# Kernel optimization log

Hardware: AMD Instinct MI355X
Metric: run time of the kernel (lower is better)

Reference implementation:

```python
import jax, jax.numpy as jnp
import numpy as np

N, E, G = 50000, 800000, 1024
IN, HID, H, L = 128, 128, 4, 3
C = HID // H  # per-head channels = 32
NEG_SLOPE = 0.2
BN_EPS = 1e-5


def setup_inputs() -> dict:
    key = jax.random.key(0)
    ks = jax.random.split(key, 12)
    s = 0.05
    x = jax.random.normal(ks[0], (N, IN), dtype=jnp.float32)
    edge_index = jax.random.randint(ks[1], (2, E), 0, N, dtype=jnp.int32)
    batch = jnp.sort(jax.random.randint(ks[2], (N,), 0, G, dtype=jnp.int32))
    # GATConv params per layer (in_dim == hidden_dim so all layers stack)
    Ws = jax.random.normal(ks[3], (L, HID, HID), dtype=jnp.float32) * s
    att_src = jax.random.normal(ks[4], (L, H, C), dtype=jnp.float32) * s
    att_dst = jax.random.normal(ks[5], (L, H, C), dtype=jnp.float32) * s
    biases = jax.random.normal(ks[6], (L, HID), dtype=jnp.float32) * s
    gammas = jnp.ones((L, HID), dtype=jnp.float32)
    betas = jnp.zeros((L, HID), dtype=jnp.float32)
    lin1_w = jax.random.normal(ks[7], (HID, HID // 2), dtype=jnp.float32) * s
    lin1_b = jnp.zeros((HID // 2,), dtype=jnp.float32)
    lin2_w = jax.random.normal(ks[8], (HID // 2, 1), dtype=jnp.float32) * s
    lin2_b = jnp.zeros((1,), dtype=jnp.float32)
    return dict(x=x, edge_index=edge_index, batch=batch, Ws=Ws, att_src=att_src,
                att_dst=att_dst, biases=biases, gammas=gammas, betas=betas,
                lin1_w=lin1_w, lin1_b=lin1_b, lin2_w=lin2_w, lin2_b=lin2_b)


def _gat_layer(x, src, dst, W, a_src, a_dst, bias):
    h = (x @ W).reshape(N, H, C)                      # [N,H,C]
    e_src = jnp.einsum('nhc,hc->nh', h, a_src)        # [N,H]
    e_dst = jnp.einsum('nhc,hc->nh', h, a_dst)
    e = jax.nn.leaky_relu(e_src[src] + e_dst[dst], NEG_SLOPE)  # [E',H]
    m = jax.ops.segment_max(e, dst, num_segments=N)   # segment softmax over dst
    ex = jnp.exp(e - m[dst])
    den = jax.ops.segment_sum(ex, dst, num_segments=N)
    alpha = ex / (den[dst] + 1e-16)
    msg = h[src] * alpha[:, :, None]                  # [E',H,C]
    out = jax.ops.segment_sum(msg, dst, num_segments=N).reshape(N, HID)
    return out + bias


def reference(x, edge_index, batch, Ws, att_src, att_dst, biases, gammas, betas,
              lin1_w, lin1_b, lin2_w, lin2_b):
    loop = jnp.arange(N, dtype=edge_index.dtype)      # add_self_loops=True
    src = jnp.concatenate([edge_index[0], loop])
    dst = jnp.concatenate([edge_index[1], loop])
    for l in range(L):
        h = _gat_layer(x, src, dst, Ws[l], att_src[l], att_dst[l], biases[l])
        mean = h.mean(axis=0)                         # BatchNorm1d (batch stats)
        var = h.var(axis=0)
        h = (h - mean) / jnp.sqrt(var + BN_EPS) * gammas[l] + betas[l]
        x = jax.nn.elu(h)
    cnt = jax.ops.segment_sum(jnp.ones((N,), x.dtype), batch, num_segments=G)
    pooled = jax.ops.segment_sum(x, batch, num_segments=G) / jnp.maximum(cnt, 1.0)[:, None]
    h1 = jax.nn.relu(pooled @ lin1_w + lin1_b)
    return (h1 @ lin2_w + lin2_b)[:, 0]               # [G]
```

## Files before the change

### kernel.cpp

```cpp
#include <hip/hip_runtime.h>
#include <hip/hip_fp16.h>
#include <math.h>

#define NN 50000
#define EE 800000
#define GG 1024
#define HIDD 128
#define NHEAD 4
#define EPTOT (EE + NN)
#define NEG_SLOPE 0.2f
#define NB ((NN + 255) / 256)
#define NTILE (NN / 16)

#define BSHIFT 9
#define NBUK 98
#define PCHUNK 4096
#define BCAP 10240

typedef _Float16 f16x8 __attribute__((ext_vector_type(8)));
typedef float f32x4 __attribute__((ext_vector_type(4)));

__global__ void zero_kernel(float* __restrict__ p, int n) {
  int i = blockIdx.x * blockDim.x + threadIdx.x;
  if (i < n) p[i] = 0.f;
}

__global__ void count_kernel(const int* __restrict__ ei, int* __restrict__ deg) {
  int e = blockIdx.x * blockDim.x + threadIdx.x;
  if (e >= EPTOT) return;
  int d = (e < EE) ? ei[EE + e] : (e - EE);
  atomicAdd(&deg[d], 1);
}

__global__ __launch_bounds__(256) void degsum_kernel(const int* __restrict__ deg,
                                                     int* __restrict__ bsum) {
  __shared__ int sh[256];
  int i = blockIdx.x * 256 + threadIdx.x;
  sh[threadIdx.x] = (i < NN) ? deg[i] : 0;
  __syncthreads();
  for (int off = 128; off > 0; off >>= 1) {
    if (threadIdx.x < off) sh[threadIdx.x] += sh[threadIdx.x + off];
    __syncthreads();
  }
  if (threadIdx.x == 0) bsum[blockIdx.x] = sh[0];
}

__global__ __launch_bounds__(256) void scanb_kernel(const int* __restrict__ bsum,
                                                    int* __restrict__ boff,
                                                    int* __restrict__ rowptr) {
  __shared__ int sh[256];
  int t = threadIdx.x;
  int v = (t < NB) ? bsum[t] : 0;
  sh[t] = v;
  __syncthreads();
  for (int off = 1; off < 256; off <<= 1) {
    int u = (t >= off) ? sh[t - off] : 0;
    __syncthreads();
    sh[t] += u;
    __syncthreads();
  }
  if (t < NB) boff[t] = sh[t] - v;
  if (t == 255) rowptr[NN] = sh[255];
}

__global__ __launch_bounds__(256) void rowptr_kernel(const int* __restrict__ deg,
                                                     const int* __restrict__ boff,
                                                     int* __restrict__ rowptr) {
  __shared__ int sh[256];
  int t = threadIdx.x;
  int i = blockIdx.x * 256 + t;
  int v = (i < NN) ? deg[i] : 0;
  sh[t] = v;
  __syncthreads();
  for (int off = 1; off < 256; off <<= 1) {
    int u = (t >= off) ? sh[t - off] : 0;
    __syncthreads();
    sh[t] += u;
    __syncthreads();
  }
  if (i < NN) rowptr[i] = boff[blockIdx.x] + sh[t] - v;
}

__global__ void bcurinit_kernel(const int* __restrict__ rowptr, int* __restrict__ bcur) {
  int b = threadIdx.x;
  if (b < NBUK) bcur[b] = rowptr[b << BSHIFT];
}

__global__ __launch_bounds__(256) void partA_kernel(const int* __restrict__ ei,
                                                    int* __restrict__ bcur,
                                                    unsigned long long* __restrict__ pairs) {
  __shared__ int hist[NBUK];
  __shared__ int sbase[NBUK];
  int t = threadIdx.x;
  if (t < NBUK) hist[t] = 0;
  __syncthreads();
  int e0 = blockIdx.x * PCHUNK;
  int ss[16], dd[16];
  int cnt = 0;
#pragma unroll
  for (int i = 0; i < 16; ++i) {
    int e = e0 + i * 256 + t;
    if (e < EPTOT) {
      int s, d;
      if (e < EE) { s = ei[e]; d = ei[EE + e]; } else { s = e - EE; d = s; }
      ss[cnt] = s; dd[cnt] = d; ++cnt;
      atomicAdd(&hist[d >> BSHIFT], 1);
    }
  }
  __syncthreads();
  if (t < NBUK) {
    int h = hist[t];
    sbase[t] = h ? atomicAdd(&bcur[t], h) : 0;
    hist[t] = 0;
  }
  __syncthreads();
  for (int i = 0; i < cnt; ++i) {
    int b = dd[i] >> BSHIFT;
    int pos = sbase[b] + atomicAdd(&hist[b], 1);
    pairs[pos] = ((unsigned long long)(unsigned)dd[i] << 32) | (unsigned)ss[i];
  }
}

__global__ __launch_bounds__(512) void partB_kernel(const unsigned long long* __restrict__ pairs,
                                                    const int* __restrict__ rowptr,
                                                    int* __restrict__ colb) {
  __shared__ int cur[512];
  __shared__ int stage[BCAP];
  int b = blockIdx.x;
  int t = threadIdx.x;
  int node0 = b << BSHIFT;
  int node1 = min(node0 + 512, NN);
  int base = rowptr[node0];
  int nE = rowptr[node1] - base;
  cur[t] = (node0 + t < node1) ? (rowptr[node0 + t] - base) : 0;
  __syncthreads();
  for (int j = t; j < nE; j += 512) {
    unsigned long long p = pairs[base + j];
    int d = (int)(p >> 32);
    int s = (int)(p & 0xffffffffu);
    int pl = atomicAdd(&cur[d - node0], 1);
    if (pl < BCAP) stage[pl] = s;
    else colb[base + pl] = s;
  }
  __syncthreads();
  int lim = min(nE, BCAP);
  for (int j = t; j < lim; j += 512) colb[base + j] = stage[j];
}

__device__ inline float bnelu1(float v, float scale, float shift) {
  v = v * scale + shift;
  return (v > 0.f) ? v : expm1f(v);
}

__global__ __launch_bounds__(256) void prepack_kernel(const float* __restrict__ Ws,
                                                      _Float16* __restrict__ Wp) {
  int f = blockIdx.x * 256 + threadIdx.x;
  if (f >= 3 * 2048) return;
  int layer = f >> 11, r = f & 2047;
  int ctile = r >> 8, ks = (r >> 6) & 3, lane = r & 63;
  const float* W = Ws + (size_t)layer * HIDD * HIDD;
  int col = ctile * 16 + (lane & 15);
  int krow = ks * 32 + (lane >> 4) * 8;
  f16x8 v;
#pragma unroll
  for (int j = 0; j < 8; ++j) v[j] = (_Float16)W[(krow + j) * HIDD + col];
  *(f16x8*)(Wp + (size_t)f * 8) = v;
}

__global__ void bnfinal_kernel(const float* __restrict__ stat,
                               const float* __restrict__ gamma,
                               const float* __restrict__ beta,
                               float* __restrict__ scsh) {
  int c = threadIdx.x;
  const float invN = 1.f / (float)NN;
  float mean = stat[c] * invN;
  float var = stat[128 + c] * invN - mean * mean;
  float scale = gamma[c] * rsqrtf(var + 1e-5f);
  scsh[c] = scale;
  scsh[128 + c] = beta[c] - mean * scale;
}

__global__ __launch_bounds__(256) void gemm_mfma_kernel(
    const float* __restrict__ Xf, const __half* __restrict__ Xh,
    const _Float16* __restrict__ Wp, const float* __restrict__ scsh,
    const float* __restrict__ asrc, const float* __restrict__ adst,
    __half* __restrict__ Hh, float* __restrict__ esrc, float* __restrict__ edst) {
  int wave = threadIdx.x >> 6, lane = threadIdx.x & 63;
  int jt = blockIdx.x * 4 + wave;
  if (jt >= NTILE) return;
  int nl = lane & 15, kg = lane >> 4;
  int node = jt * 16 + nl;
  f32x4 acc[8];
#pragma unroll
  for (int c = 0; c < 8; ++c) acc[c] = (f32x4){0.f, 0.f, 0.f, 0.f};
#pragma unroll
  for (int ks = 0; ks < 4; ++ks) {
    int k0 = ks * 32 + kg * 8;
    f16x8 bfrag;
    if (Xf) {
      const float* xrow = Xf + (size_t)node * HIDD;
      float4 va = *(const float4*)(xrow + k0);
      float4 vb = *(const float4*)(xrow + k0 + 4);
      bfrag[0] = (_Float16)va.x; bfrag[1] = (_Float16)va.y;
      bfrag[2] = (_Float16)va.z; bfrag[3] = (_Float16)va.w;
      bfrag[4] = (_Float16)vb.x; bfrag[5] = (_Float16)vb.y;
      bfrag[6] = (_Float16)vb.z; bfrag[7] = (_Float16)vb.w;
    } else {
      const __half2* xrow = (const __half2*)(Xh + (size_t)node * HIDD + k0);
      float4 s0 = *(const float4*)(scsh + k0);
      float4 s1 = *(const float4*)(scsh + k0 + 4);
      float4 t0 = *(const float4*)(scsh + HIDD + k0);
      float4 t1 = *(const float4*)(scsh + HIDD + k0 + 4);
      float2 f0 = __half22float2(xrow[0]);
      float2 f1 = __half22float2(xrow[1]);
      float2 f2 = __half22float2(xrow[2]);
      float2 f3 = __half22float2(xrow[3]);
      bfrag[0] = (_Float16)bnelu1(f0.x, s0.x, t0.x);
      bfrag[1] = (_Float16)bnelu1(f0.y, s0.y, t0.y);
      bfrag[2] = (_Float16)bnelu1(f1.x, s0.z, t0.z);
      bfrag[3] = (_Float16)bnelu1(f1.y, s0.w, t0.w);
      bfrag[4] = (_Float16)bnelu1(f2.x, s1.x, t1.x);
      bfrag[5] = (_Float16)bnelu1(f2.y, s1.y, t1.y);
      bfrag[6] = (_Float16)bnelu1(f3.x, s1.z, t1.z);
      bfrag[7] = (_Float16)bnelu1(f3.y, s1.w, t1.w);
    }
#pragma unroll
    for (int c = 0; c < 8; ++c) {
      f16x8 afrag = *(const f16x8*)(Wp + (((size_t)(c * 4 + ks) * 64 + lane) << 3));
      acc[c] = __builtin_amdgcn_mfma_f32_16x16x32_f16(afrag, bfrag, acc[c], 0, 0, 0);
    }
  }
  float es_p[4] = {0.f, 0.f, 0.f, 0.f};
  float ed_p[4] = {0.f, 0.f, 0.f, 0.f};
  __half* hrow = Hh + (size_t)node * HIDD;
#pragma unroll
  for (int c = 0; c < 8; ++c) {
    int ch0 = c * 16 + kg * 4;
    __half2 h01 = __floats2half2_rn(acc[c][0], acc[c][1]);
    __half2 h23 = __floats2half2_rn(acc[c][2], acc[c][3]);
    union { __half2 h[2]; float2 f; } u;
    u.h[0] = h01; u.h[1] = h23;
    *(float2*)(hrow + ch0) = u.f;
    float4 av = *(const float4*)(asrc + ch0);
    float4 bv = *(const float4*)(adst + ch0);
    int hd = c >> 1;
    es_p[hd] += acc[c][0] * av.x + acc[c][1] * av.y + acc[c][2] * av.z + acc[c][3] * av.w;
    ed_p[hd] += acc[c][0] * bv.x + acc[c][1] * bv.y + acc[c][2] * bv.z + acc[c][3] * bv.w;
  }
#pragma unroll
  for (int hd = 0; hd < 4; ++hd) {
    es_p[hd] += __shfl_xor(es_p[hd], 16);
    es_p[hd] += __shfl_xor(es_p[hd], 32);
    ed_p[hd] += __shfl_xor(ed_p[hd], 16);
    ed_p[hd] += __shfl_xor(ed_p[hd], 32);
  }
  float es_o = (kg == 0) ? es_p[0] : (kg == 1) ? es_p[1] : (kg == 2) ? es_p[2] : es_p[3];
  float ed_o = (kg == 0) ? ed_p[0] : (kg == 1) ? ed_p[1] : (kg == 2) ? ed_p[2] : ed_p[3];
  esrc[node * 4 + kg] = es_o;
  edst[node * 4 + kg] = ed_o;
}

__global__ __launch_bounds__(256) void agg_kernel(const __half2* __restrict__ Hh,
                                                  const float* __restrict__ esrc,
                                                  const float* __restrict__ edst,
                                                  const int* __restrict__ rowptr,
                                                  const int* __restrict__ colb,
                                                  const float* __restrict__ bias,
                                                  __half* __restrict__ outh) {
  int wid = (blockIdx.x * 256 + threadIdx.x) >> 6;
  int lane = threadIdx.x & 63;
  if (wid >= NN) return;
  int hd = lane >> 4;
  float ed = edst[wid * 4 + hd];
  int e0 = rowptr[wid], e1 = rowptr[wid + 1];
  float den = 0.f, ax = 0.f, ay = 0.f;
  const __half2* hbase = Hh + lane;
  int e = e0;
  for (; e + 4 <= e1; e += 4) {
    int s[4];
#pragma unroll
    for (int j = 0; j < 4; ++j) s[j] = colb[e + j];
    float es[4];
    __half2 hv[4];
#pragma unroll
    for (int j = 0; j < 4; ++j) {
      es[j] = esrc[s[j] * 4 + hd];
      hv[j] = hbase[(size_t)s[j] * 64];
    }
#pragma unroll
    for (int j = 0; j < 4; ++j) {
      float z = es[j] + ed;
      z = fmaxf(z, NEG_SLOPE * z);
      float w = __expf(z);
      float2 f = __half22float2(hv[j]);
      den += w;
      ax += w * f.x;
      ay += w * f.y;
    }
  }
  for (; e < e1; ++e) {
    int src = colb[e];
    float esv = esrc[src * 4 + hd];
    __half2 hvv = hbase[(size_t)src * 64];
    float z = esv + ed;
    z = fmaxf(z, NEG_SLOPE * z);
    float w = __expf(z);
    float2 f = __half22float2(hvv);
    den += w;
    ax += w * f.x;
    ay += w * f.y;
  }
  float inv = 1.f / (den + 1e-16f);
  int c = 2 * lane;
  float vx = ax * inv + bias[c];
  float vy = ay * inv + bias[c + 1];
  *((__half2*)(outh + (size_t)wid * HIDD) + lane) = __floats2half2_rn(vx, vy);
}

__global__ __launch_bounds__(256) void bnstat_kernel(const __half* __restrict__ X,
                                                     float* __restrict__ stat) {
  __shared__ float sh[256];
  int tid = threadIdx.x;
  int c = tid & 127;
  int half = tid >> 7;
  float s = 0.f, q = 0.f;
  for (int r = blockIdx.x * 2 + half; r < NN; r += gridDim.x * 2) {
    float v = __half2float(X[(size_t)r * HIDD + c]);
    s += v;
    q += v * v;
  }
  sh[tid] = s;
  __syncthreads();
  if (tid < 128) atomicAdd(&stat[c], s + sh[tid + 128]);
  __syncthreads();
  sh[tid] = q;
  __syncthreads();
  if (tid < 128) atomicAdd(&stat[128 + c], q + sh[tid + 128]);
}

__global__ void gbound_kernel(const int* __restrict__ batch, int* __restrict__ gstart) {
  int i = blockIdx.x * blockDim.x + threadIdx.x;
  if (i >= NN) return;
  int cur = batch[i];
  int prev = (i == 0) ? -1 : batch[i - 1];
  for (int g = prev + 1; g <= cur; ++g) gstart[g] = i;
  if (i == NN - 1) {
    for (int g = cur + 1; g <= GG; ++g) gstart[g] = NN;
  }
}

__global__ __launch_bounds__(128) void pool_kernel(const __half* __restrict__ X,
                                                   const int* __restrict__ gstart,
                                                   const float* __restrict__ scsh,
                                                   float* __restrict__ pooled) {
  int g = blockIdx.x;
  int c = threadIdx.x;
  float scale = scsh[c];
  float shift = scsh[128 + c];
  int n0 = gstart[g], n1 = gstart[g + 1];
  float s = 0.f;
  for (int n = n0; n < n1; ++n)
    s += bnelu1(__half2float(X[(size_t)n * HIDD + c]), scale, shift);
  float inv = (n1 > n0) ? 1.f / (float)(n1 - n0) : 0.f;
  pooled[(size_t)g * HIDD + c] = s * inv;
}

__global__ __launch_bounds__(256) void head_kernel(const float* __restrict__ pooled,
                                                   const float* __restrict__ w1,
                                                   const float* __restrict__ b1,
                                                   const float* __restrict__ w2,
                                                   const float* __restrict__ b2,
                                                   float* __restrict__ out) {
  int wid = (blockIdx.x * 256 + threadIdx.x) >> 6;
  int lane = threadIdx.x & 63;
  if (wid >= GG) return;
  float acc = b1[lane];
  const float* pg = pooled + (size_t)wid * HIDD;
  for (int k = 0; k < HIDD; ++k) {
    acc += pg[k] * w1[k * 64 + lane];
  }
  acc = fmaxf(acc, 0.f);
  float v = acc * w2[lane];
#pragma unroll
  for (int off = 32; off > 0; off >>= 1) v += __shfl_down(v, off);
  if (lane == 0) out[wid] = v + b2[0];
}

extern "C" void kernel_launch(void* const* d_in, const int* in_sizes, int n_in,
                              void* d_out, int out_size, void* d_ws, size_t ws_size,
                              hipStream_t stream) {
  const float* x    = (const float*)d_in[0];
  const int* ei     = (const int*)d_in[1];
  const int* batch  = (const int*)d_in[2];
  const float* Ws   = (const float*)d_in[3];
  const float* asrc = (const float*)d_in[4];
  const float* adst = (const float*)d_in[5];
  const float* bias = (const float*)d_in[6];
  const float* gam  = (const float*)d_in[7];
  const float* bet  = (const float*)d_in[8];
  const float* w1   = (const float*)d_in[9];
  const float* b1   = (const float*)d_in[10];
  const float* w2   = (const float*)d_in[11];
  const float* b2   = (const float*)d_in[12];
  float* out = (float*)d_out;

  char* wp = (char*)d_ws;
  auto carve = [&](size_t bytes) -> char* {
    char* p = wp;
    wp += (bytes + 255) & ~(size_t)255;
    return p;
  };
  __half* B     = (__half*)carve((size_t)NN * HIDD * 2);
  __half* Hh    = (__half*)carve((size_t)NN * HIDD * 2);
  _Float16* Wp  = (_Float16*)carve((size_t)3 * HIDD * HIDD * 2);
  float* scsh   = (float*)carve((size_t)3 * 256 * 4);
  float* esrc   = (float*)carve((size_t)NN * NHEAD * 4);
  float* edst   = (float*)carve((size_t)NN * NHEAD * 4);
  int* rowptr   = (int*)carve((size_t)(NN + 1) * 4);
  int* colb     = (int*)carve((size_t)EPTOT * 4);
  unsigned long long* pairs = (unsigned long long*)carve((size_t)EPTOT * 8);
  int* bcur     = (int*)carve((size_t)NBUK * 4);
  int* bsum     = (int*)carve((size_t)NB * 4);
  int* boff     = (int*)carve((size_t)NB * 4);
  int* gstart   = (int*)carve((size_t)(GG + 1) * 4);
  float* pooled = (float*)carve((size_t)GG * HIDD * 4);
  char* z0 = wp;
  int* deg      = (int*)carve((size_t)NN * 4);
  float* stats  = (float*)carve(768 * 4);
  int zcount = (int)((wp - z0) / 4);

  zero_kernel<<<(zcount + 255) / 256, 256, 0, stream>>>((float*)z0, zcount);
  prepack_kernel<<<24, 256, 0, stream>>>(Ws, Wp);
  count_kernel<<<(EPTOT + 255) / 256, 256, 0, stream>>>(ei, deg);
  degsum_kernel<<<NB, 256, 0, stream>>>(deg, bsum);
  scanb_kernel<<<1, 256, 0, stream>>>(bsum, boff, rowptr);
  rowptr_kernel<<<NB, 256, 0, stream>>>(deg, boff, rowptr);
  bcurinit_kernel<<<1, 128, 0, stream>>>(rowptr, bcur);
  partA_kernel<<<(EPTOT + PCHUNK - 1) / PCHUNK, 256, 0, stream>>>(ei, bcur, pairs);
  partB_kernel<<<NBUK, 512, 0, stream>>>(pairs, rowptr, colb);
  gbound_kernel<<<(NN + 255) / 256, 256, 0, stream>>>(batch, gstart);

  for (int l = 0; l < 3; ++l) {
    const float* sc_prev = (l == 0) ? nullptr : scsh + (l - 1) * 256;
    const float* xf = (l == 0) ? x : nullptr;
    const __half* xh = (l == 0) ? nullptr : B;
    gemm_mfma_kernel<<<(NTILE + 3) / 4, 256, 0, stream>>>(
        xf, xh, Wp + (size_t)l * HIDD * HIDD, sc_prev,
        asrc + l * NHEAD * 32, adst + l * NHEAD * 32, Hh, esrc, edst);
    agg_kernel<<<(NN * 64 + 255) / 256, 256, 0, stream>>>(
        (const __half2*)Hh, esrc, edst, rowptr, colb, bias + l * HIDD, B);
    bnstat_kernel<<<1024, 256, 0, stream>>>(B, stats + l * 256);
    bnfinal_kernel<<<1, 128, 0, stream>>>(stats + l * 256, gam + l * HIDD,
                                          bet + l * HIDD, scsh + l * 256);
  }
  pool_kernel<<<GG, 128, 0, stream>>>(B, gstart, scsh + 2 * 256, pooled);
  head_kernel<<<(GG * 64 + 255) / 256, 256, 0, stream>>>(pooled, w1, b1, w2, b2, out);
}
```

Before: 407.0 us.

## Fuse pool and head, fold bcur init into scan, unroll aggregation with exp2

Merges the pooling and MLP head kernels into one per-graph kernel, and computes bucket cursors inside the block-offset scan to drop the separate bcurinit launch. Pre-scales the attention logits by log2(e) so the aggregation kernel can use exp2f. It also adds an 8-wide unrolled edge loop to raise memory-level parallelism. Narrows 64-bit index math to 32-bit and loads the half-precision input row as one 16-byte vector. These cut launch overhead and address arithmetic, at the cost of more registers in the aggregation loop.

```diff
diff --git a/kernel.cpp b/kernel.cpp
--- a/kernel.cpp
+++ b/kernel.cpp
@@ -11,6 +11,7 @@
 #define NEG_SLOPE 0.2f
 #define NB ((NN + 255) / 256)
 #define NTILE (NN / 16)
+#define LOG2E 1.4426950408889634f
 
 #define BSHIFT 9
 #define NBUK 98
@@ -47,7 +48,8 @@
 
 __global__ __launch_bounds__(256) void scanb_kernel(const int* __restrict__ bsum,
                                                     int* __restrict__ boff,
-                                                    int* __restrict__ rowptr) {
+                                                    int* __restrict__ rowptr,
+                                                    int* __restrict__ bcur) {
   __shared__ int sh[256];
   int t = threadIdx.x;
   int v = (t < NB) ? bsum[t] : 0;
@@ -60,6 +62,7 @@
     __syncthreads();
   }
   if (t < NB) boff[t] = sh[t] - v;
+  if (!(t & 1) && (t >> 1) < NBUK) bcur[t >> 1] = sh[t] - v;
   if (t == 255) rowptr[NN] = sh[255];
 }
 
@@ -79,11 +82,6 @@
     __syncthreads();
   }
   if (i < NN) rowptr[i] = boff[blockIdx.x] + sh[t] - v;
-}
-
-__global__ void bcurinit_kernel(const int* __restrict__ rowptr, int* __restrict__ bcur) {
-  int b = threadIdx.x;
-  if (b < NBUK) bcur[b] = rowptr[b << BSHIFT];
 }
 
 __global__ __launch_bounds__(256) void partA_kernel(const int* __restrict__ ei,
@@ -164,7 +162,7 @@
   f16x8 v;
 #pragma unroll
   for (int j = 0; j < 8; ++j) v[j] = (_Float16)W[(krow + j) * HIDD + col];
-  *(f16x8*)(Wp + (size_t)f * 8) = v;
+  *(f16x8*)(Wp + f * 8) = v;
 }
 
 __global__ void bnfinal_kernel(const float* __restrict__ stat,
@@ -198,7 +196,7 @@
     int k0 = ks * 32 + kg * 8;
     f16x8 bfrag;
     if (Xf) {
-      const float* xrow = Xf + (size_t)node * HIDD;
+      const float* xrow = Xf + node * HIDD;
       float4 va = *(const float4*)(xrow + k0);
       float4 vb = *(const float4*)(xrow + k0 + 4);
       bfrag[0] = (_Float16)va.x; bfrag[1] = (_Float16)va.y;
@@ -206,15 +204,16 @@
       bfrag[4] = (_Float16)vb.x; bfrag[5] = (_Float16)vb.y;
       bfrag[6] = (_Float16)vb.z; bfrag[7] = (_Float16)vb.w;
     } else {
-      const __half2* xrow = (const __half2*)(Xh + (size_t)node * HIDD + k0);
+      float4 raw = *(const float4*)(Xh + node * HIDD + k0);
+      const __half2* hp = (const __half2*)&raw;
       float4 s0 = *(const float4*)(scsh + k0);
       float4 s1 = *(const float4*)(scsh + k0 + 4);
       float4 t0 = *(const float4*)(scsh + HIDD + k0);
       float4 t1 = *(const float4*)(scsh + HIDD + k0 + 4);
-      float2 f0 = __half22float2(xrow[0]);
-      float2 f1 = __half22float2(xrow[1]);
-      float2 f2 = __half22float2(xrow[2]);
-      float2 f3 = __half22float2(xrow[3]);
+      float2 f0 = __half22float2(hp[0]);
+      float2 f1 = __half22float2(hp[1]);
+      float2 f2 = __half22float2(hp[2]);
+      float2 f3 = __half22float2(hp[3]);
       bfrag[0] = (_Float16)bnelu1(f0.x, s0.x, t0.x);
       bfrag[1] = (_Float16)bnelu1(f0.y, s0.y, t0.y);
       bfrag[2] = (_Float16)bnelu1(f1.x, s0.z, t0.z);
@@ -226,13 +225,13 @@
     }
 #pragma unroll
     for (int c = 0; c < 8; ++c) {
-      f16x8 afrag = *(const f16x8*)(Wp + (((size_t)(c * 4 + ks) * 64 + lane) << 3));
+      f16x8 afrag = *(const f16x8*)(Wp + (((c * 4 + ks) * 64 + lane) << 3));
       acc[c] = __builtin_amdgcn_mfma_f32_16x16x32_f16(afrag, bfrag, acc[c], 0, 0, 0);
     }
   }
   float es_p[4] = {0.f, 0.f, 0.f, 0.f};
   float ed_p[4] = {0.f, 0.f, 0.f, 0.f};
-  __half* hrow = Hh + (size_t)node * HIDD;
+  __half* hrow = Hh + node * HIDD;
 #pragma unroll
   for (int c = 0; c < 8; ++c) {
     int ch0 = c * 16 + kg * 4;
@@ -256,8 +255,8 @@
   }
   float es_o = (kg == 0) ? es_p[0] : (kg == 1) ? es_p[1] : (kg == 2) ? es_p[2] : es_p[3];
   float ed_o = (kg == 0) ? ed_p[0] : (kg == 1) ? ed_p[1] : (kg == 2) ? ed_p[2] : ed_p[3];
-  esrc[node * 4 + kg] = es_o;
-  edst[node * 4 + kg] = ed_o;
+  esrc[node * 4 + kg] = es_o * LOG2E;
+  edst[node * 4 + kg] = ed_o * LOG2E;
 }
 
 __global__ __launch_bounds__(256) void agg_kernel(const __half2* __restrict__ Hh,
@@ -274,8 +273,27 @@
   float ed = edst[wid * 4 + hd];
   int e0 = rowptr[wid], e1 = rowptr[wid + 1];
   float den = 0.f, ax = 0.f, ay = 0.f;
-  const __half2* hbase = Hh + lane;
   int e = e0;
+  for (; e + 8 <= e1; e += 8) {
+    int s[8];
+#pragma unroll
+    for (int j = 0; j < 8; ++j) s[j] = colb[e + j];
+    float es[8];
+    __half2 hv[8];
+#pragma unroll
+    for (int j = 0; j < 8; ++j) {
+      es[j] = esrc[s[j] * 4 + hd];
+      hv[j] = Hh[s[j] * 64 + lane];
+    }
+#pragma unroll
+    for (int j = 0; j < 8; ++j) {
+      float z = es[j] + ed;
+      z = fmaxf(z, NEG_SLOPE * z);
+      float w = exp2f(z);
+      float2 f = __half22float2(hv[j]);
+      den += w; ax += w * f.x; ay += w * f.y;
+    }
+  }
   for (; e + 4 <= e1; e += 4) {
     int s[4];
 #pragma unroll
@@ -285,36 +303,32 @@
 #pragma unroll
     for (int j = 0; j < 4; ++j) {
       es[j] = esrc[s[j] * 4 + hd];
-      hv[j] = hbase[(size_t)s[j] * 64];
+      hv[j] = Hh[s[j] * 64 + lane];
     }
 #pragma unroll
     for (int j = 0; j < 4; ++j) {
       float z = es[j] + ed;
       z = fmaxf(z, NEG_SLOPE * z);
-      float w = __expf(z);
+      float w = exp2f(z);
       float2 f = __half22float2(hv[j]);
-      den += w;
-      ax += w * f.x;
-      ay += w * f.y;
+      den += w; ax += w * f.x; ay += w * f.y;
     }
   }
   for (; e < e1; ++e) {
     int src = colb[e];
     float esv = esrc[src * 4 + hd];
-    __half2 hvv = hbase[(size_t)src * 64];
+    __half2 hvv = Hh[src * 64 + lane];
     float z = esv + ed;
     z = fmaxf(z, NEG_SLOPE * z);
-    float w = __expf(z);
+    float w = exp2f(z);
     float2 f = __half22float2(hvv);
-    den += w;
-    ax += w * f.x;
-    ay += w * f.y;
+    den += w; ax += w * f.x; ay += w * f.y;
   }
   float inv = 1.f / (den + 1e-16f);
   int c = 2 * lane;
   float vx = ax * inv + bias[c];
   float vy = ay * inv + bias[c + 1];
-  *((__half2*)(outh + (size_t)wid * HIDD) + lane) = __floats2half2_rn(vx, vy);
+  ((__half2*)outh)[wid * 64 + lane] = __floats2half2_rn(vx, vy);
 }
 
 __global__ __launch_bounds__(256) void bnstat_kernel(const __half* __restrict__ X,
@@ -325,7 +339,7 @@
   int half = tid >> 7;
   float s = 0.f, q = 0.f;
   for (int r = blockIdx.x * 2 + half; r < NN; r += gridDim.x * 2) {
-    float v = __half2float(X[(size_t)r * HIDD + c]);
+    float v = __half2float(X[r * HIDD + c]);
     s += v;
     q += v * v;
   }
@@ -349,10 +363,15 @@
   }
 }
 
-__global__ __launch_bounds__(128) void pool_kernel(const __half* __restrict__ X,
-                                                   const int* __restrict__ gstart,
-                                                   const float* __restrict__ scsh,
-                                                   float* __restrict__ pooled) {
+__global__ __launch_bounds__(128) void poolhead_kernel(const __half* __restrict__ X,
+                                                       const int* __restrict__ gstart,
+                                                       const float* __restrict__ scsh,
+                                                       const float* __restrict__ w1,
+                                                       const float* __restrict__ b1,
+                                                       const float* __restrict__ w2,
+                                                       const float* __restrict__ b2,
+                                                       float* __restrict__ out) {
+  __shared__ float pl[HIDD];
   int g = blockIdx.x;
   int c = threadIdx.x;
   float scale = scsh[c];
@@ -360,30 +379,20 @@
   int n0 = gstart[g], n1 = gstart[g + 1];
   float s = 0.f;
   for (int n = n0; n < n1; ++n)
-    s += bnelu1(__half2float(X[(size_t)n * HIDD + c]), scale, shift);
+    s += bnelu1(__half2float(X[n * HIDD + c]), scale, shift);
   float inv = (n1 > n0) ? 1.f / (float)(n1 - n0) : 0.f;
-  pooled[(size_t)g * HIDD + c] = s * inv;
-}
-
-__global__ __launch_bounds__(256) void head_kernel(const float* __restrict__ pooled,
-                                                   const float* __restrict__ w1,
-                                                   const float* __restrict__ b1,
-                                                   const float* __restrict__ w2,
-                                                   const float* __restrict__ b2,
-                                                   float* __restrict__ out) {
-  int wid = (blockIdx.x * 256 + threadIdx.x) >> 6;
-  int lane = threadIdx.x & 63;
-  if (wid >= GG) return;
-  float acc = b1[lane];
-  const float* pg = pooled + (size_t)wid * HIDD;
-  for (int k = 0; k < HIDD; ++k) {
-    acc += pg[k] * w1[k * 64 + lane];
-  }
-  acc = fmaxf(acc, 0.f);
-  float v = acc * w2[lane];
-#pragma unroll
-  for (int off = 32; off > 0; off >>= 1) v += __shfl_down(v, off);
-  if (lane == 0) out[wid] = v + b2[0];
+  pl[c] = s * inv;
+  __syncthreads();
+  if (c < 64) {
+    float acc = b1[c];
+#pragma unroll 4
+    for (int k = 0; k < HIDD; ++k) acc += pl[k] * w1[k * 64 + c];
+    acc = fmaxf(acc, 0.f);
+    float v = acc * w2[c];
+#pragma unroll
+    for (int off = 32; off > 0; off >>= 1) v += __shfl_down(v, off);
+    if (c == 0) out[g] = v + b2[0];
+  }
 }
 
 extern "C" void kernel_launch(void* const* d_in, const int* in_sizes, int n_in,
@@ -423,7 +432,6 @@
   int* bsum     = (int*)carve((size_t)NB * 4);
   int* boff     = (int*)carve((size_t)NB * 4);
   int* gstart   = (int*)carve((size_t)(GG + 1) * 4);
-  float* pooled = (float*)carve((size_t)GG * HIDD * 4);
   char* z0 = wp;
   int* deg      = (int*)carve((size_t)NN * 4);
   float* stats  = (float*)carve(768 * 4);
@@ -433,9 +441,8 @@
   prepack_kernel<<<24, 256, 0, stream>>>(Ws, Wp);
   count_kernel<<<(EPTOT + 255) / 256, 256, 0, stream>>>(ei, deg);
   degsum_kernel<<<NB, 256, 0, stream>>>(deg, bsum);
-  scanb_kernel<<<1, 256, 0, stream>>>(bsum, boff, rowptr);
+  scanb_kernel<<<1, 256, 0, stream>>>(bsum, boff, rowptr, bcur);
   rowptr_kernel<<<NB, 256, 0, stream>>>(deg, boff, rowptr);
-  bcurinit_kernel<<<1, 128, 0, stream>>>(rowptr, bcur);
   partA_kernel<<<(EPTOT + PCHUNK - 1) / PCHUNK, 256, 0, stream>>>(ei, bcur, pairs);
   partB_kernel<<<NBUK, 512, 0, stream>>>(pairs, rowptr, colb);
   gbound_kernel<<<(NN + 255) / 256, 256, 0, stream>>>(batch, gstart);
@@ -453,6 +460,5 @@
     bnfinal_kernel<<<1, 128, 0, stream>>>(stats + l * 256, gam + l * HIDD,
                                           bet + l * HIDD, scsh + l * 256);
   }
-  pool_kernel<<<GG, 128, 0, stream>>>(B, gstart, scsh + 2 * 256, pooled);
-  head_kernel<<<(GG * 64 + 255) / 256, 256, 0, stream>>>(pooled, w1, b1, w2, b2, out);
-}
+  poolhead_kernel<<<GG, 128, 0, stream>>>(B, gstart, scsh + 2 * 256, w1, b1, w2, b2, out);
+}
```

New measurement: 392.6 us. -3.5%, faster.
